# Performance work log

Hardware: AMD Instinct MI355X
Metric: run time of the kernel (lower is better)

The kernel has to match this reference:

```python
import jax, jax.numpy as jnp
import numpy as np

TEMP = 0.5  # init kwarg `tmp`
NUM_CLASSES = 100


def setup_inputs() -> dict:
    key = jax.random.key(0)
    k1, k2 = jax.random.split(key)
    embedding = jax.random.normal(k1, (8192, 256), dtype=jnp.float32)
    label = jax.random.randint(k2, (8192,), 0, NUM_CLASSES, dtype=jnp.int64)
    return {"embedding": embedding, "label": label}


def reference(embedding, label):
    # Row-normalize -> pairwise cosine similarity [N, N]
    normed = embedding / jnp.linalg.norm(embedding, axis=1, keepdims=True)
    sim = (normed @ normed.T) / TEMP  # already divided by temperature

    N = embedding.shape[0]
    eye = jnp.eye(N, dtype=bool)

    # Denominator: sum of exp(sim) over off-diagonal entries per row
    exp_sim = jnp.exp(sim)
    row_sum = jnp.sum(jnp.where(eye, 0.0, exp_sim), axis=1)  # [N]

    # log(exp(sim_ij) / row_sum_i) = sim_ij - log(row_sum_i)
    log_prob = sim - jnp.log(row_sum)[:, None]

    # Positive mask: same label, i != j
    pos_mask = (label[:, None] == label[None, :]) & ~eye
    n_i = jnp.sum(pos_mask, axis=1)  # positives per anchor

    inner = jnp.sum(jnp.where(pos_mask, log_prob, 0.0), axis=1)  # [N]
    per_anchor = jnp.where(n_i > 0, -inner / jnp.maximum(n_i, 1).astype(sim.dtype), 0.0)
    return jnp.sum(per_anchor)
```

## Files before the change

kernel.cpp:

```cpp
#include <hip/hip_runtime.h>
#include <hip/hip_bf16.h>
#include <stdint.h>

#define N    8192
#define D    256
#define NCLS 100

static constexpr float TEMP    = 0.5f;
static constexpr float SCALE_F = 1.69864360f;
static constexpr float E2      = 7.38905609893065f;
static constexpr float LN2     = 0.69314718055994531f;

typedef __bf16 bf16x8 __attribute__((ext_vector_type(8)));
typedef float  f32x4  __attribute__((ext_vector_type(4)));

__device__ __forceinline__ unsigned short f2bf(float f) {
  union { float f; unsigned int u; } x; x.f = f;
  unsigned int r = x.u + 0x7fffu + ((x.u >> 16) & 1u);
  return (unsigned short)(r >> 16);
}
__device__ __forceinline__ float bf2f(unsigned short b) {
  union { unsigned int u; float f; } x; x.u = ((unsigned int)b) << 16;
  return x.f;
}
__device__ __forceinline__ void gld16(const void* g, void* l) {
  __builtin_amdgcn_global_load_lds(
      (const __attribute__((address_space(1))) unsigned int*)g,
      (__attribute__((address_space(3))) unsigned int*)l, 16, 0, 0);
}

__global__ __launch_bounds__(256) void normalize_kernel(
    const float* __restrict__ emb, const long long* __restrict__ label,
    unsigned short* __restrict__ abf, int* __restrict__ cnt,
    int* __restrict__ list) {
  const int row  = blockIdx.x * 4 + (threadIdx.x >> 6);
  const int lane = threadIdx.x & 63;
  const float4 v = ((const float4*)(emb + (size_t)row * D))[lane];
  float ss = v.x * v.x + v.y * v.y + v.z * v.z + v.w * v.w;
#pragma unroll
  for (int off = 1; off < 64; off <<= 1) ss += __shfl_xor(ss, off);
  const float s = rsqrtf(ss) * SCALE_F;
  ushort4 o;
  o.x = f2bf(v.x * s); o.y = f2bf(v.y * s);
  o.z = f2bf(v.z * s); o.w = f2bf(v.w * s);
  ((ushort4*)(abf + (size_t)row * D))[lane] = o;
  if (lane == 0) {
    const int c = (int)label[row];
    const int slot = atomicAdd(cnt + c, 1);
    list[c * 256 + slot] = row;
  }
}

#define TM 128

__global__ __launch_bounds__(256) void simexp_rowsum_kernel(
    const unsigned short* __restrict__ A, float* __restrict__ rowsum) {
  __shared__ __align__(16) unsigned short sb[TM * D];
  const int tid  = threadIdx.x;
  const int w    = tid >> 6;
  const int lane = tid & 63;
  const int quad = lane >> 4;
  const int l15  = lane & 15;

  const int id = blockIdx.x;
  int bi = (int)((129.0f - sqrtf(16641.0f - 8.0f * (float)id)) * 0.5f);
  while (bi > 0 && (bi * (129 - bi)) / 2 > id) --bi;
  while (((bi + 1) * (128 - bi)) / 2 <= id) ++bi;
  const int bj   = bi + (id - (bi * (129 - bi)) / 2);
  const int row0 = bi * TM;
  const int jb0  = bj * TM;
  const bool diag = (bi == bj);

  bf16x8 af[2][8];
#pragma unroll
  for (int mt = 0; mt < 2; ++mt)
#pragma unroll
    for (int ks = 0; ks < 8; ++ks)
      af[mt][ks] = *(const bf16x8*)(
          A + (size_t)(row0 + w * 32 + mt * 16 + l15) * D + ks * 32 + quad * 8);

  {
    const int b = lane & 31;
    const int g = b >> 3;
    const int h = lane >> 5;
#pragma unroll
    for (int t = 0; t < 16; ++t) {
      const int r = (t * 4 + w) * 2 + h;
      const int src =
          (jb0 + r) * D + g * 64 + (((b & 7) ^ (r & 7)) << 3);
      gld16(A + src, sb + (t * 4 + w) * 512);
    }
  }
  __syncthreads();

  f32x4 acc[2][8];
#pragma unroll
  for (int mt = 0; mt < 2; ++mt)
#pragma unroll
    for (int nt = 0; nt < 8; ++nt) acc[mt][nt] = (f32x4){0.f, 0.f, 0.f, 0.f};

#pragma unroll
  for (int ks = 0; ks < 8; ++ks) {
    bf16x8 bfr[8];
#pragma unroll
    for (int nt = 0; nt < 8; ++nt) {
      const int n = nt * 16 + l15;
      const int c = ((ks & 1) * 4 + quad) ^ (l15 & 7);
      bfr[nt] = *(const bf16x8*)(sb + n * D + (ks >> 1) * 64 + c * 8);
    }
#pragma unroll
    for (int mt = 0; mt < 2; ++mt)
#pragma unroll
      for (int nt = 0; nt < 8; ++nt)
        acc[mt][nt] = __builtin_amdgcn_mfma_f32_16x16x32_bf16(
            af[mt][ks], bfr[nt], acc[mt][nt], 0, 0, 0);
  }

  float cs[8];
#pragma unroll
  for (int nt = 0; nt < 8; ++nt) cs[nt] = 0.f;
#pragma unroll
  for (int mt = 0; mt < 2; ++mt) {
    float rp[4] = {0.f, 0.f, 0.f, 0.f};
#pragma unroll
    for (int nt = 0; nt < 8; ++nt)
#pragma unroll
      for (int e = 0; e < 4; ++e) {
        const float v = __builtin_amdgcn_exp2f(acc[mt][nt][e]);
        rp[e] += v;
        cs[nt] += v;
      }
#pragma unroll
    for (int e = 0; e < 4; ++e) {
      float v = rp[e];
      v += __shfl_xor(v, 1);
      v += __shfl_xor(v, 2);
      v += __shfl_xor(v, 4);
      v += __shfl_xor(v, 8);
      if (l15 == 0)
        atomicAdd(&rowsum[row0 + w * 32 + mt * 16 + quad * 4 + e], v);
    }
  }

  if (!diag) {
    float* cred = (float*)sb;
    __syncthreads();
#pragma unroll
    for (int nt = 0; nt < 8; ++nt) {
      float v = cs[nt];
      v += __shfl_xor(v, 16);
      v += __shfl_xor(v, 32);
      if (quad == 0) cred[w * 128 + nt * 16 + l15] = v;
    }
    __syncthreads();
    if (tid < 128)
      atomicAdd(&rowsum[jb0 + tid],
                cred[tid] + cred[128 + tid] + cred[256 + tid] +
                    cred[384 + tid]);
  }
}

__global__ __launch_bounds__(256) void finalize_kernel(
    const unsigned short* __restrict__ abf, const float* __restrict__ rowsum,
    const long long* __restrict__ label, const int* __restrict__ cnt,
    const int* __restrict__ list, float* __restrict__ out) {
  __shared__ float red[4];
  __shared__ int rows_l[256];
  const int tid  = threadIdx.x;
  const int w    = tid >> 6;
  const int lane = tid & 63;

  if (blockIdx.x < NCLS) {
    const int c = blockIdx.x;
    const int m = cnt[c];
    if (m <= 1) return;
    if (tid < m) rows_l[tid] = list[c * 256 + tid];
    __syncthreads();
    float acc = 0.f;
    for (int s = 0; s < m; ++s)
      acc += bf2f(abf[(size_t)rows_l[s] * D + tid]);
    float v = acc * acc;
#pragma unroll
    for (int off = 1; off < 64; off <<= 1) v += __shfl_xor(v, off);
    if (lane == 0) red[w] = v;
    __syncthreads();
    if (tid == 0) {
      const float ssq = red[0] + red[1] + red[2] + red[3];
      const float term = (ssq * LN2 - 2.0f * (float)m) / (float)(m - 1);
      atomicAdd(out, -term);
    }
  } else {
    const int i = (blockIdx.x - NCLS) * 256 + tid;
    const int c = (int)label[i];
    float v = 0.f;
    if (cnt[c] > 1)
      v = __builtin_amdgcn_logf(rowsum[i] - E2) * LN2;
#pragma unroll
    for (int off = 1; off < 64; off <<= 1) v += __shfl_xor(v, off);
    if (lane == 0) red[w] = v;
    __syncthreads();
    if (tid == 0)
      atomicAdd(out, red[0] + red[1] + red[2] + red[3]);
  }
}

extern "C" void kernel_launch(void* const* d_in, const int* in_sizes, int n_in,
                              void* d_out, int out_size, void* d_ws,
                              size_t ws_size, hipStream_t stream) {
  const float* emb = (const float*)d_in[0];
  const long long* label = (const long long*)d_in[1];
  float* out = (float*)d_out;

  char* ws = (char*)d_ws;
  unsigned short* abf = (unsigned short*)ws;
  float* rowsum = (float*)(ws + (size_t)N * D * 2);
  int* cnt = (int*)(rowsum + N);
  int* list = cnt + 128;

  hipMemsetAsync(rowsum, 0, (size_t)N * 4 + 128 * 4, stream);
  hipMemsetAsync(out, 0, sizeof(float), stream);

  normalize_kernel<<<N / 4, 256, 0, stream>>>(emb, label, abf, cnt, list);

  simexp_rowsum_kernel<<<2080, 256, 0, stream>>>(abf, rowsum);

  finalize_kernel<<<NCLS + N / 256, 256, 0, stream>>>(abf, rowsum, label, cnt,
                                                      list, out);
}
```

Baseline: 137.9 us.

## Load B fragments directly from global memory into registers, dropping LDS staging

The 64KB LDS staging of the B tile through global_load_lds and the block-wide barrier are removed. Each wave now loads its B fragments straight from global (L2) memory into registers, double-buffered across k-steps, and LDS is kept only for the small column-sum reduction. Shrinking LDS from 64KB to 2KB is meant to raise occupancy and remove the barrier stall. In exchange, all four waves redundantly fetch the same B tile from cache and lose the swizzled LDS reuse, which raises L2 traffic.

```diff
diff --git a/kernel.cpp b/kernel.cpp
--- a/kernel.cpp
+++ b/kernel.cpp
@@ -22,11 +22,6 @@
 __device__ __forceinline__ float bf2f(unsigned short b) {
   union { unsigned int u; float f; } x; x.u = ((unsigned int)b) << 16;
   return x.f;
-}
-__device__ __forceinline__ void gld16(const void* g, void* l) {
-  __builtin_amdgcn_global_load_lds(
-      (const __attribute__((address_space(1))) unsigned int*)g,
-      (__attribute__((address_space(3))) unsigned int*)l, 16, 0, 0);
 }
 
 __global__ __launch_bounds__(256) void normalize_kernel(
@@ -55,7 +50,7 @@
 
 __global__ __launch_bounds__(256) void simexp_rowsum_kernel(
     const unsigned short* __restrict__ A, float* __restrict__ rowsum) {
-  __shared__ __align__(16) unsigned short sb[TM * D];
+  __shared__ float cred[4][128];
   const int tid  = threadIdx.x;
   const int w    = tid >> 6;
   const int lane = tid & 63;
@@ -71,27 +66,16 @@
   const int jb0  = bj * TM;
   const bool diag = (bi == bj);
 
+  const unsigned short* Abase =
+      A + (size_t)(row0 + w * 32 + l15) * D + quad * 8;
   bf16x8 af[2][8];
 #pragma unroll
   for (int mt = 0; mt < 2; ++mt)
 #pragma unroll
     for (int ks = 0; ks < 8; ++ks)
-      af[mt][ks] = *(const bf16x8*)(
-          A + (size_t)(row0 + w * 32 + mt * 16 + l15) * D + ks * 32 + quad * 8);
-
-  {
-    const int b = lane & 31;
-    const int g = b >> 3;
-    const int h = lane >> 5;
-#pragma unroll
-    for (int t = 0; t < 16; ++t) {
-      const int r = (t * 4 + w) * 2 + h;
-      const int src =
-          (jb0 + r) * D + g * 64 + (((b & 7) ^ (r & 7)) << 3);
-      gld16(A + src, sb + (t * 4 + w) * 512);
-    }
-  }
-  __syncthreads();
+      af[mt][ks] = *(const bf16x8*)(Abase + mt * 16 * D + ks * 32);
+
+  const unsigned short* Bbase = A + (size_t)(jb0 + l15) * D + quad * 8;
 
   f32x4 acc[2][8];
 #pragma unroll
@@ -99,21 +83,26 @@
 #pragma unroll
     for (int nt = 0; nt < 8; ++nt) acc[mt][nt] = (f32x4){0.f, 0.f, 0.f, 0.f};
 
+  bf16x8 b0[8], b1[8];
+#pragma unroll
+  for (int nt = 0; nt < 8; ++nt)
+    b0[nt] = *(const bf16x8*)(Bbase + nt * 16 * D);
 #pragma unroll
   for (int ks = 0; ks < 8; ++ks) {
-    bf16x8 bfr[8];
+    bf16x8* cur = (ks & 1) ? b1 : b0;
+    bf16x8* nxt = (ks & 1) ? b0 : b1;
+    if (ks < 7) {
+#pragma unroll
+      for (int nt = 0; nt < 8; ++nt)
+        nxt[nt] = *(const bf16x8*)(Bbase + nt * 16 * D + (ks + 1) * 32);
+    }
 #pragma unroll
     for (int nt = 0; nt < 8; ++nt) {
-      const int n = nt * 16 + l15;
-      const int c = ((ks & 1) * 4 + quad) ^ (l15 & 7);
-      bfr[nt] = *(const bf16x8*)(sb + n * D + (ks >> 1) * 64 + c * 8);
-    }
-#pragma unroll
-    for (int mt = 0; mt < 2; ++mt)
-#pragma unroll
-      for (int nt = 0; nt < 8; ++nt)
-        acc[mt][nt] = __builtin_amdgcn_mfma_f32_16x16x32_bf16(
-            af[mt][ks], bfr[nt], acc[mt][nt], 0, 0, 0);
+      acc[0][nt] = __builtin_amdgcn_mfma_f32_16x16x32_bf16(af[0][ks], cur[nt],
+                                                           acc[0][nt], 0, 0, 0);
+      acc[1][nt] = __builtin_amdgcn_mfma_f32_16x16x32_bf16(af[1][ks], cur[nt],
+                                                           acc[1][nt], 0, 0, 0);
+    }
   }
 
   float cs[8];
@@ -143,20 +132,17 @@
   }
 
   if (!diag) {
-    float* cred = (float*)sb;
-    __syncthreads();
 #pragma unroll
     for (int nt = 0; nt < 8; ++nt) {
       float v = cs[nt];
       v += __shfl_xor(v, 16);
       v += __shfl_xor(v, 32);
-      if (quad == 0) cred[w * 128 + nt * 16 + l15] = v;
+      if (quad == 0) cred[w][nt * 16 + l15] = v;
     }
     __syncthreads();
     if (tid < 128)
       atomicAdd(&rowsum[jb0 + tid],
-                cred[tid] + cred[128 + tid] + cred[256 + tid] +
-                    cred[384 + tid]);
+                cred[0][tid] + cred[1][tid] + cred[2][tid] + cred[3][tid]);
   }
 }
 
```

New measurement: 186.9 us. 35.5% more time.
